# Kernel tuning notes

Hardware: AMD Instinct MI355X
Metric: run time of the kernel (lower is better)

Reference implementation:

```python
import jax, jax.numpy as jnp
import numpy as np

B, T, D = 64, 2048, 300

def setup_inputs() -> dict:
    key = jax.random.key(0)
    k1, k2, k3, k4 = jax.random.split(key, 4)
    gate_encoding = jax.random.uniform(k1, (B, T, D), dtype=jnp.float32)
    inputs_encoding = jax.random.normal(k2, (B, T, D), dtype=jnp.float32)
    # kaiming-normal-ish init: std = sqrt(2 / fan_in)
    std = float(np.sqrt(2.0 / D))
    Wz = jax.random.normal(k3, (D, D), dtype=jnp.float32) * std
    Wo = jax.random.normal(k4, (D, D), dtype=jnp.float32) * std
    bz = jnp.zeros((D,), dtype=jnp.float32)
    bo = jnp.zeros((D,), dtype=jnp.float32)
    return {"gate_encoding": gate_encoding, "inputs_encoding": inputs_encoding,
            "Wz": Wz, "bz": bz, "Wo": Wo, "bo": bo}

def reference(gate_encoding, inputs_encoding, Wz, bz, Wo, bo):
    # Batch the two linear projections across all timesteps (torch.nn.Linear: x @ W.T + b)
    z = jnp.tanh(jnp.einsum('btd,ed->bte', inputs_encoding, Wz) + bz)  # [B,T,D]
    o = jnp.tanh(jnp.einsum('btd,ed->bte', inputs_encoding, Wo) + bo)  # [B,T,D]

    # Sequential gated recurrence: c_t = g_t * c_{t-1} + (1 - g_t) * z_t ; h_t = o_t * c_t
    def step(c, gz_o):
        g_t, z_t, o_t = gz_o
        c = g_t * c + (1.0 - g_t) * z_t
        return c, o_t * c

    c0 = jnp.zeros((gate_encoding.shape[0], gate_encoding.shape[2]), dtype=inputs_encoding.dtype)
    # scan over time: move T to leading axis
    _, h = jax.lax.scan(step, c0,
                        (jnp.swapaxes(gate_encoding, 0, 1),
                         jnp.swapaxes(z, 0, 1),
                         jnp.swapaxes(o, 0, 1)))
    return jnp.swapaxes(h, 0, 1)  # [B,T,D]
```

## Files before the change

kernel.cpp:

```cpp
#include <hip/hip_runtime.h>
#include <hip/hip_bf16.h>

typedef _Float16 f16x8 __attribute__((ext_vector_type(8)));
typedef _Float16 f16x4 __attribute__((ext_vector_type(4)));
typedef float f32x4 __attribute__((ext_vector_type(4)));

#define B_SZ 64
#define T_SZ 2048
#define D_SZ 300
#define M_SZ (B_SZ * T_SZ)
#define KP 320
#define NP 640
#define NCHUNK 32
#define CLEN 64

__device__ __forceinline__ void gld_lds16(const void* g, void* l) {
    __builtin_amdgcn_global_load_lds(
        (const __attribute__((address_space(1))) unsigned int*)g,
        (__attribute__((address_space(3))) unsigned int*)l,
        16, 0, 0);
}

__device__ __forceinline__ float fast_tanh(float x) {
    float e = __expf(2.0f * x);
    return 1.0f - 2.0f * __builtin_amdgcn_rcpf(e + 1.0f);
}

__global__ void pack_x(const float* __restrict__ in, _Float16* __restrict__ out) {
    unsigned int i = blockIdx.x * 256u + threadIdx.x;
    f32x4 v = *(const f32x4*)(in + (size_t)i * 4);
#pragma unroll
    for (int j = 0; j < 4; ++j) {
        unsigned int f = i * 4 + j;
        unsigned int row = f / D_SZ;
        unsigned int k = f - row * D_SZ;
        out[(size_t)row * KP + k] = (_Float16)v[j];
    }
}

__global__ void pad_x(_Float16* __restrict__ out) {
    unsigned int i = blockIdx.x * 256u + threadIdx.x;
    unsigned int j = i * 4;
    unsigned int row = j / 20;
    unsigned int k0 = j - row * 20;
    f16x4 z = {};
    *(f16x4*)(out + (size_t)row * KP + 300 + k0) = z;
}

__global__ void pack_w(const float* __restrict__ Wz, const float* __restrict__ Wo,
                       _Float16* __restrict__ W) {
    unsigned int i = blockIdx.x * 256u + threadIdx.x;
    if (i >= NP * KP) return;
    unsigned int n = i / KP;
    unsigned int k = i - n * KP;
    float v = 0.0f;
    if (k < D_SZ) {
        if (n < D_SZ) v = Wz[n * D_SZ + k];
        else if (n >= 320 && n < 320 + D_SZ) v = Wo[(n - 320) * D_SZ + k];
    }
    W[i] = (_Float16)v;
}

__global__ void pack_bias(const float* __restrict__ bz, const float* __restrict__ bo,
                          float* __restrict__ bias) {
    int n = threadIdx.x;
    float v = 0.0f;
    if (n < D_SZ) v = bz[n];
    else if (n >= 320 && n < 320 + D_SZ) v = bo[n - 320];
    bias[n] = v;
}

__global__ __launch_bounds__(256) void gemm_zo(const _Float16* __restrict__ X,
                                               const _Float16* __restrict__ W,
                                               const float* __restrict__ bias,
                                               _Float16* __restrict__ C) {
    __shared__ _Float16 As[3][128 * 32];
    __shared__ _Float16 Bs[3][128 * 32];

    const int tid = threadIdx.x;
    const int lane = tid & 63;
    const int wid = tid >> 6;
    const int wm = wid >> 1, wn = wid & 1;

    int g = blockIdx.x;
    int s = (g & 7) * (5120 / 8) + (g >> 3);
    int bm = s / 5;
    int bn = s - bm * 5;

    f32x4 acc[4][4] = {};

    const int r_in_c = lane >> 2;
    const int u_phys = lane & 3;

    const _Float16* Abase = X + (size_t)(bm * 128) * KP;
    const _Float16* Bbase = W + (size_t)(bn * 128) * KP;

    auto stage = [&](int buf, int kt) {
#pragma unroll
        for (int j = 0; j < 2; ++j) {
            int c = wid + j * 4;
            int row = c * 16 + r_in_c;
            int ul = u_phys ^ ((row >> 1) & 3);
            gld_lds16(Abase + (size_t)row * KP + kt * 32 + ul * 8, &As[buf][c * 512]);
            gld_lds16(Bbase + (size_t)row * KP + kt * 32 + ul * 8, &Bs[buf][c * 512]);
        }
    };

    stage(0, 0);
    stage(1, 1);

#pragma unroll 1
    for (int kt = 0; kt < 10; ++kt) {
        if (kt < 8) {
            stage((kt + 2) % 3, kt + 2);
            asm volatile("s_waitcnt vmcnt(8)" ::: "memory");
        } else if (kt == 8) {
            asm volatile("s_waitcnt vmcnt(4)" ::: "memory");
        } else {
            asm volatile("s_waitcnt vmcnt(0)" ::: "memory");
        }
        __builtin_amdgcn_s_barrier();
        __builtin_amdgcn_sched_barrier(0);

        const int cb = kt % 3;
        f16x8 bf[4], af[4];
#pragma unroll
        for (int ns = 0; ns < 4; ++ns) {
            int row = wn * 64 + ns * 16 + (lane & 15);
            int u = (lane >> 4) ^ ((row >> 1) & 3);
            bf[ns] = *(const f16x8*)&Bs[cb][row * 32 + u * 8];
        }
#pragma unroll
        for (int ms = 0; ms < 4; ++ms) {
            int row = wm * 64 + ms * 16 + (lane & 15);
            int u = (lane >> 4) ^ ((row >> 1) & 3);
            af[ms] = *(const f16x8*)&As[cb][row * 32 + u * 8];
        }
        asm volatile("s_waitcnt lgkmcnt(0)" ::: "memory");
        __builtin_amdgcn_s_barrier();
        __builtin_amdgcn_sched_barrier(0);

        __builtin_amdgcn_s_setprio(1);
#pragma unroll
        for (int ms = 0; ms < 4; ++ms)
#pragma unroll
            for (int ns = 0; ns < 4; ++ns)
                acc[ms][ns] = __builtin_amdgcn_mfma_f32_16x16x32_f16(bf[ns], af[ms], acc[ms][ns], 0, 0, 0);
        __builtin_amdgcn_s_setprio(0);
    }

    const int mrow0 = bm * 128 + wm * 64;
    const int ncol0 = bn * 128 + wn * 64;
#pragma unroll
    for (int ns = 0; ns < 4; ++ns) {
        int nb = ncol0 + ns * 16 + (lane >> 4) * 4;
        f32x4 b4 = *(const f32x4*)&bias[nb];
#pragma unroll
        for (int ms = 0; ms < 4; ++ms) {
            int m = mrow0 + ms * 16 + (lane & 15);
            f16x4 v;
#pragma unroll
            for (int r = 0; r < 4; ++r)
                v[r] = (_Float16)fast_tanh(acc[ms][ns][r] + b4[r]);
            *(f16x4*)&C[(size_t)m * NP + nb] = v;
        }
    }
}

__global__ void scan_p1(const float* __restrict__ gate, const _Float16* __restrict__ C,
                        float* __restrict__ Aout, float* __restrict__ Bout) {
    int b = blockIdx.x >> 5;
    int nc = blockIdx.x & 31;
    int d = threadIdx.x;
    if (d >= D_SZ) return;
    size_t base = (size_t)b * T_SZ + (size_t)nc * CLEN;
    const float* gp = gate + base * D_SZ + d;
    const _Float16* zp = C + base * NP + d;
    float A = 1.0f, Bc = 0.0f;
    for (int t = 0; t < CLEN; ++t) {
        float gv = gp[(size_t)t * D_SZ];
        float zv = (float)zp[(size_t)t * NP];
        A *= gv;
        Bc = gv * Bc + (1.0f - gv) * zv;
    }
    int o = (b * NCHUNK + nc) * D_SZ + d;
    Aout[o] = A;
    Bout[o] = Bc;
}

__global__ void scan_p2(const float* __restrict__ A, const float* __restrict__ Bc,
                        float* __restrict__ Cin) {
    int idx = blockIdx.x * 256 + threadIdx.x;
    if (idx >= B_SZ * D_SZ) return;
    int b = idx / D_SZ;
    int d = idx - b * D_SZ;
    float c = 0.0f;
    for (int nc = 0; nc < NCHUNK; ++nc) {
        int o = (b * NCHUNK + nc) * D_SZ + d;
        Cin[o] = c;
        c = A[o] * c + Bc[o];
    }
}

__global__ void scan_p3(const float* __restrict__ gate, const _Float16* __restrict__ C,
                        const float* __restrict__ Cin, float* __restrict__ out) {
    int b = blockIdx.x >> 5;
    int nc = blockIdx.x & 31;
    int d = threadIdx.x;
    if (d >= D_SZ) return;
    size_t base = (size_t)b * T_SZ + (size_t)nc * CLEN;
    const float* gp = gate + base * D_SZ + d;
    const _Float16* zp = C + base * NP + d;
    const _Float16* op = zp + 320;
    float* hp = out + base * D_SZ + d;
    float c = Cin[(b * NCHUNK + nc) * D_SZ + d];
    for (int t = 0; t < CLEN; ++t) {
        float gv = gp[(size_t)t * D_SZ];
        float zv = (float)zp[(size_t)t * NP];
        float ov = (float)op[(size_t)t * NP];
        c = gv * c + (1.0f - gv) * zv;
        hp[(size_t)t * D_SZ] = ov * c;
    }
}

extern "C" void kernel_launch(void* const* d_in, const int* in_sizes, int n_in,
                              void* d_out, int out_size, void* d_ws, size_t ws_size,
                              hipStream_t stream) {
    const float* gate = (const float*)d_in[0];
    const float* xin  = (const float*)d_in[1];
    const float* Wz   = (const float*)d_in[2];
    const float* bz   = (const float*)d_in[3];
    const float* Wo   = (const float*)d_in[4];
    const float* bo   = (const float*)d_in[5];
    float* out = (float*)d_out;

    char* ws = (char*)d_ws;
    _Float16* Xf16 = (_Float16*)(ws);
    _Float16* C16  = (_Float16*)(ws + 83886080ull);
    _Float16* Wc   = (_Float16*)(ws + 251658240ull);
    float*    bias = (float*)   (ws + 252067840ull);
    float*    Ach  = (float*)   (ws);
    float*    Bch  = (float*)   (ws + 2457600ull);
    float*    Cin  = (float*)   (ws + 4915200ull);

    pack_x<<<(M_SZ * D_SZ / 4) / 256, 256, 0, stream>>>(xin, Xf16);
    pad_x<<<(M_SZ * 20 / 4) / 256, 256, 0, stream>>>(Xf16);
    pack_w<<<(NP * KP + 255) / 256, 256, 0, stream>>>(Wz, Wo, Wc);
    pack_bias<<<1, NP, 0, stream>>>(bz, bo, bias);

    gemm_zo<<<(M_SZ / 128) * (NP / 128), 256, 0, stream>>>(Xf16, Wc, bias, C16);

    scan_p1<<<B_SZ * NCHUNK, 320, 0, stream>>>(gate, C16, Ach, Bch);
    scan_p2<<<(B_SZ * D_SZ + 255) / 256, 256, 0, stream>>>(Ach, Bch, Cin);
    scan_p3<<<B_SZ * NCHUNK, 320, 0, stream>>>(gate, C16, Cin, out);
}
```

Measured before the change: 327.4 us.

## Fuse fp32-to-fp16 input conversion into GEMM with direct register loads

Drops the separate pack_x and pad_x kernels. The GEMM now reads fp32 X directly from global memory into registers and converts it to fp16 on the fly, masking the K tail past 300. The LDS staging, swizzling and barriers are replaced by per-wave register double-buffered global loads. This removes a full write and read pass of the packed f16 input. In exchange, the GEMM reads twice as many bytes per A element, waves sharing the same rows load them redundantly, and it loses LDS-based reuse.

```diff
diff --git a/kernel.cpp b/kernel.cpp
--- a/kernel.cpp
+++ b/kernel.cpp
@@ -14,37 +14,9 @@
 #define NCHUNK 32
 #define CLEN 64
 
-__device__ __forceinline__ void gld_lds16(const void* g, void* l) {
-    __builtin_amdgcn_global_load_lds(
-        (const __attribute__((address_space(1))) unsigned int*)g,
-        (__attribute__((address_space(3))) unsigned int*)l,
-        16, 0, 0);
-}
-
 __device__ __forceinline__ float fast_tanh(float x) {
     float e = __expf(2.0f * x);
     return 1.0f - 2.0f * __builtin_amdgcn_rcpf(e + 1.0f);
-}
-
-__global__ void pack_x(const float* __restrict__ in, _Float16* __restrict__ out) {
-    unsigned int i = blockIdx.x * 256u + threadIdx.x;
-    f32x4 v = *(const f32x4*)(in + (size_t)i * 4);
-#pragma unroll
-    for (int j = 0; j < 4; ++j) {
-        unsigned int f = i * 4 + j;
-        unsigned int row = f / D_SZ;
-        unsigned int k = f - row * D_SZ;
-        out[(size_t)row * KP + k] = (_Float16)v[j];
-    }
-}
-
-__global__ void pad_x(_Float16* __restrict__ out) {
-    unsigned int i = blockIdx.x * 256u + threadIdx.x;
-    unsigned int j = i * 4;
-    unsigned int row = j / 20;
-    unsigned int k0 = j - row * 20;
-    f16x4 z = {};
-    *(f16x4*)(out + (size_t)row * KP + 300 + k0) = z;
 }
 
 __global__ void pack_w(const float* __restrict__ Wz, const float* __restrict__ Wo,
@@ -70,16 +42,33 @@
     bias[n] = v;
 }
 
-__global__ __launch_bounds__(256) void gemm_zo(const _Float16* __restrict__ X,
+__device__ __forceinline__ f16x8 cvt8(f32x4 v0, f32x4 v1) {
+    f16x8 r;
+    r[0] = (_Float16)v0[0]; r[1] = (_Float16)v0[1];
+    r[2] = (_Float16)v0[2]; r[3] = (_Float16)v0[3];
+    r[4] = (_Float16)v1[0]; r[5] = (_Float16)v1[1];
+    r[6] = (_Float16)v1[2]; r[7] = (_Float16)v1[3];
+    return r;
+}
+
+__device__ __forceinline__ f16x8 loadA(const float* __restrict__ p, bool tail, int kq) {
+    f32x4 v0 = {}, v1 = {};
+    if (!tail) {
+        v0 = *(const f32x4*)p;
+        v1 = *(const f32x4*)(p + 4);
+    } else {
+        if (kq < 2) v0 = *(const f32x4*)p;
+        if (kq < 1) v1 = *(const f32x4*)(p + 4);
+    }
+    return cvt8(v0, v1);
+}
+
+__global__ __launch_bounds__(256) void gemm_zo(const float* __restrict__ X,
                                                const _Float16* __restrict__ W,
                                                const float* __restrict__ bias,
                                                _Float16* __restrict__ C) {
-    __shared__ _Float16 As[3][128 * 32];
-    __shared__ _Float16 Bs[3][128 * 32];
-
-    const int tid = threadIdx.x;
-    const int lane = tid & 63;
-    const int wid = tid >> 6;
+    const int lane = threadIdx.x & 63;
+    const int wid = threadIdx.x >> 6;
     const int wm = wid >> 1, wn = wid & 1;
 
     int g = blockIdx.x;
@@ -87,77 +76,66 @@
     int bm = s / 5;
     int bn = s - bm * 5;
 
+    const int l15 = lane & 15;
+    const int kq = lane >> 4;
+
+    const float* ap[4];
+    const _Float16* bp[4];
+#pragma unroll
+    for (int ms = 0; ms < 4; ++ms) {
+        int row = bm * 128 + wm * 64 + ms * 16 + l15;
+        ap[ms] = X + (size_t)row * D_SZ + kq * 8;
+    }
+#pragma unroll
+    for (int ns = 0; ns < 4; ++ns) {
+        int row = bn * 128 + wn * 64 + ns * 16 + l15;
+        bp[ns] = W + (size_t)row * KP + kq * 8;
+    }
+
     f32x4 acc[4][4] = {};
 
-    const int r_in_c = lane >> 2;
-    const int u_phys = lane & 3;
-
-    const _Float16* Abase = X + (size_t)(bm * 128) * KP;
-    const _Float16* Bbase = W + (size_t)(bn * 128) * KP;
-
-    auto stage = [&](int buf, int kt) {
-#pragma unroll
-        for (int j = 0; j < 2; ++j) {
-            int c = wid + j * 4;
-            int row = c * 16 + r_in_c;
-            int ul = u_phys ^ ((row >> 1) & 3);
-            gld_lds16(Abase + (size_t)row * KP + kt * 32 + ul * 8, &As[buf][c * 512]);
-            gld_lds16(Bbase + (size_t)row * KP + kt * 32 + ul * 8, &Bs[buf][c * 512]);
+    f16x8 ac[4], bc[4];
+#pragma unroll
+    for (int ms = 0; ms < 4; ++ms) ac[ms] = loadA(ap[ms], false, kq);
+#pragma unroll
+    for (int ns = 0; ns < 4; ++ns) bc[ns] = *(const f16x8*)(bp[ns]);
+
+#pragma unroll 2
+    for (int kt = 0; kt < 10; ++kt) {
+        f16x8 an[4], bnx[4];
+        if (kt < 9) {
+            bool tail = (kt == 8);
+#pragma unroll
+            for (int ms = 0; ms < 4; ++ms) an[ms] = loadA(ap[ms] + (kt + 1) * 32, tail, kq);
+#pragma unroll
+            for (int ns = 0; ns < 4; ++ns) bnx[ns] = *(const f16x8*)(bp[ns] + (kt + 1) * 32);
         }
-    };
-
-    stage(0, 0);
-    stage(1, 1);
-
-#pragma unroll 1
-    for (int kt = 0; kt < 10; ++kt) {
-        if (kt < 8) {
-            stage((kt + 2) % 3, kt + 2);
-            asm volatile("s_waitcnt vmcnt(8)" ::: "memory");
-        } else if (kt == 8) {
-            asm volatile("s_waitcnt vmcnt(4)" ::: "memory");
-        } else {
-            asm volatile("s_waitcnt vmcnt(0)" ::: "memory");
+
+        __builtin_amdgcn_s_setprio(1);
+#pragma unroll
+        for (int ms = 0; ms < 4; ++ms)
+#pragma unroll
+            for (int ns = 0; ns < 4; ++ns)
+                acc[ms][ns] = __builtin_amdgcn_mfma_f32_16x16x32_f16(bc[ns], ac[ms], acc[ms][ns], 0, 0, 0);
+        __builtin_amdgcn_s_setprio(0);
+
+        if (kt < 9) {
+#pragma unroll
+            for (int ms = 0; ms < 4; ++ms) ac[ms] = an[ms];
+#pragma unroll
+            for (int ns = 0; ns < 4; ++ns) bc[ns] = bnx[ns];
         }
-        __builtin_amdgcn_s_barrier();
-        __builtin_amdgcn_sched_barrier(0);
-
-        const int cb = kt % 3;
-        f16x8 bf[4], af[4];
-#pragma unroll
-        for (int ns = 0; ns < 4; ++ns) {
-            int row = wn * 64 + ns * 16 + (lane & 15);
-            int u = (lane >> 4) ^ ((row >> 1) & 3);
-            bf[ns] = *(const f16x8*)&Bs[cb][row * 32 + u * 8];
-        }
-#pragma unroll
-        for (int ms = 0; ms < 4; ++ms) {
-            int row = wm * 64 + ms * 16 + (lane & 15);
-            int u = (lane >> 4) ^ ((row >> 1) & 3);
-            af[ms] = *(const f16x8*)&As[cb][row * 32 + u * 8];
-        }
-        asm volatile("s_waitcnt lgkmcnt(0)" ::: "memory");
-        __builtin_amdgcn_s_barrier();
-        __builtin_amdgcn_sched_barrier(0);
-
-        __builtin_amdgcn_s_setprio(1);
-#pragma unroll
-        for (int ms = 0; ms < 4; ++ms)
-#pragma unroll
-            for (int ns = 0; ns < 4; ++ns)
-                acc[ms][ns] = __builtin_amdgcn_mfma_f32_16x16x32_f16(bf[ns], af[ms], acc[ms][ns], 0, 0, 0);
-        __builtin_amdgcn_s_setprio(0);
     }
 
     const int mrow0 = bm * 128 + wm * 64;
     const int ncol0 = bn * 128 + wn * 64;
 #pragma unroll
     for (int ns = 0; ns < 4; ++ns) {
-        int nb = ncol0 + ns * 16 + (lane >> 4) * 4;
+        int nb = ncol0 + ns * 16 + kq * 4;
         f32x4 b4 = *(const f32x4*)&bias[nb];
 #pragma unroll
         for (int ms = 0; ms < 4; ++ms) {
-            int m = mrow0 + ms * 16 + (lane & 15);
+            int m = mrow0 + ms * 16 + l15;
             f16x4 v;
 #pragma unroll
             for (int r = 0; r < 4; ++r)
@@ -235,20 +213,17 @@
     float* out = (float*)d_out;
 
     char* ws = (char*)d_ws;
-    _Float16* Xf16 = (_Float16*)(ws);
-    _Float16* C16  = (_Float16*)(ws + 83886080ull);
-    _Float16* Wc   = (_Float16*)(ws + 251658240ull);
-    float*    bias = (float*)   (ws + 252067840ull);
-    float*    Ach  = (float*)   (ws);
-    float*    Bch  = (float*)   (ws + 2457600ull);
-    float*    Cin  = (float*)   (ws + 4915200ull);
-
-    pack_x<<<(M_SZ * D_SZ / 4) / 256, 256, 0, stream>>>(xin, Xf16);
-    pad_x<<<(M_SZ * 20 / 4) / 256, 256, 0, stream>>>(Xf16);
+    _Float16* C16  = (_Float16*)(ws);
+    _Float16* Wc   = (_Float16*)(ws + 167772160ull);
+    float*    bias = (float*)   (ws + 168181760ull);
+    float*    Ach  = (float*)   (ws + 168184320ull);
+    float*    Bch  = (float*)   (ws + 170641920ull);
+    float*    Cin  = (float*)   (ws + 173099520ull);
+
     pack_w<<<(NP * KP + 255) / 256, 256, 0, stream>>>(Wz, Wo, Wc);
     pack_bias<<<1, NP, 0, stream>>>(bz, bo, bias);
 
-    gemm_zo<<<(M_SZ / 128) * (NP / 128), 256, 0, stream>>>(Xf16, Wc, bias, C16);
+    gemm_zo<<<(M_SZ / 128) * (NP / 128), 256, 0, stream>>>(xin, Wc, bias, C16);
 
     scan_p1<<<B_SZ * NCHUNK, 320, 0, stream>>>(gate, C16, Ach, Bch);
     scan_p2<<<(B_SZ * D_SZ + 255) / 256, 256, 0, stream>>>(Ach, Bch, Cin);
```

Result: slower. 415.8 us (+27.0%).

## Merge X pack and pad kernels; stage GEMM epilogue through LDS for wide stores

Applied to the files above, without the earlier changes.

The fp16 packing of X now runs in one kernel: each thread converts a row-aligned group of four floats into an f16x4 store, or zero-fills the padding, replacing scalar half stores and a separate pad launch. The GEMM epilogue writes tanh results into a swizzled per-wave LDS tile, then reads them back as 16-byte rows, so global stores to C are coalesced 128-byte row segments instead of scattered 8-byte writes. This adds a barrier and LDS round-trips in the epilogue.

```diff
diff --git a/kernel.cpp b/kernel.cpp
--- a/kernel.cpp
+++ b/kernel.cpp
@@ -28,23 +28,18 @@
 
 __global__ void pack_x(const float* __restrict__ in, _Float16* __restrict__ out) {
     unsigned int i = blockIdx.x * 256u + threadIdx.x;
-    f32x4 v = *(const f32x4*)(in + (size_t)i * 4);
-#pragma unroll
-    for (int j = 0; j < 4; ++j) {
-        unsigned int f = i * 4 + j;
-        unsigned int row = f / D_SZ;
-        unsigned int k = f - row * D_SZ;
-        out[(size_t)row * KP + k] = (_Float16)v[j];
-    }
-}
-
-__global__ void pad_x(_Float16* __restrict__ out) {
-    unsigned int i = blockIdx.x * 256u + threadIdx.x;
-    unsigned int j = i * 4;
-    unsigned int row = j / 20;
-    unsigned int k0 = j - row * 20;
-    f16x4 z = {};
-    *(f16x4*)(out + (size_t)row * KP + 300 + k0) = z;
+    unsigned int row = i / 80;
+    unsigned int kq = i - row * 80;
+    if (kq < 75) {
+        f32x4 v = *(const f32x4*)(in + (size_t)row * D_SZ + kq * 4);
+        f16x4 h;
+#pragma unroll
+        for (int r = 0; r < 4; ++r) h[r] = (_Float16)v[r];
+        *(f16x4*)(out + (size_t)row * KP + kq * 4) = h;
+    } else {
+        f16x4 z = {};
+        *(f16x4*)(out + (size_t)row * KP + 300 + (kq - 75) * 4) = z;
+    }
 }
 
 __global__ void pack_w(const float* __restrict__ Wz, const float* __restrict__ Wo,
@@ -109,6 +104,9 @@
     stage(0, 0);
     stage(1, 1);
 
+    const int l15 = lane & 15;
+    const int kq = lane >> 4;
+
 #pragma unroll 1
     for (int kt = 0; kt < 10; ++kt) {
         if (kt < 8) {
@@ -126,14 +124,14 @@
         f16x8 bf[4], af[4];
 #pragma unroll
         for (int ns = 0; ns < 4; ++ns) {
-            int row = wn * 64 + ns * 16 + (lane & 15);
-            int u = (lane >> 4) ^ ((row >> 1) & 3);
+            int row = wn * 64 + ns * 16 + l15;
+            int u = kq ^ ((row >> 1) & 3);
             bf[ns] = *(const f16x8*)&Bs[cb][row * 32 + u * 8];
         }
 #pragma unroll
         for (int ms = 0; ms < 4; ++ms) {
-            int row = wm * 64 + ms * 16 + (lane & 15);
-            int u = (lane >> 4) ^ ((row >> 1) & 3);
+            int row = wm * 64 + ms * 16 + l15;
+            int u = kq ^ ((row >> 1) & 3);
             af[ms] = *(const f16x8*)&As[cb][row * 32 + u * 8];
         }
         asm volatile("s_waitcnt lgkmcnt(0)" ::: "memory");
@@ -149,20 +147,35 @@
         __builtin_amdgcn_s_setprio(0);
     }
 
+    __syncthreads();
+    _Float16* et = &As[0][0] + wid * 1024;
+
     const int mrow0 = bm * 128 + wm * 64;
     const int ncol0 = bn * 128 + wn * 64;
-#pragma unroll
-    for (int ns = 0; ns < 4; ++ns) {
-        int nb = ncol0 + ns * 16 + (lane >> 4) * 4;
-        f32x4 b4 = *(const f32x4*)&bias[nb];
-#pragma unroll
-        for (int ms = 0; ms < 4; ++ms) {
-            int m = mrow0 + ms * 16 + (lane & 15);
+    const int row8 = lane >> 3;
+    const int u8 = lane & 7;
+
+    f32x4 b4[4];
+#pragma unroll
+    for (int ns = 0; ns < 4; ++ns)
+        b4[ns] = *(const f32x4*)&bias[ncol0 + ns * 16 + kq * 4];
+
+#pragma unroll
+    for (int ms = 0; ms < 4; ++ms) {
+#pragma unroll
+        for (int ns = 0; ns < 4; ++ns) {
             f16x4 v;
 #pragma unroll
             for (int r = 0; r < 4; ++r)
-                v[r] = (_Float16)fast_tanh(acc[ms][ns][r] + b4[r]);
-            *(f16x4*)&C[(size_t)m * NP + nb] = v;
+                v[r] = (_Float16)fast_tanh(acc[ms][ns][r] + b4[ns][r]);
+            int up = ((ns << 1) | (kq >> 1)) ^ (l15 & 7);
+            *(f16x4*)&et[l15 * 64 + up * 8 + (kq & 1) * 4] = v;
+        }
+#pragma unroll
+        for (int j = 0; j < 2; ++j) {
+            int rr = row8 + j * 8;
+            f16x8 o = *(const f16x8*)&et[rr * 64 + (u8 ^ (rr & 7)) * 8];
+            *(f16x8*)&C[(size_t)(mrow0 + ms * 16 + rr) * NP + ncol0 + u8 * 8] = o;
         }
     }
 }
@@ -243,8 +256,7 @@
     float*    Bch  = (float*)   (ws + 2457600ull);
     float*    Cin  = (float*)   (ws + 4915200ull);
 
-    pack_x<<<(M_SZ * D_SZ / 4) / 256, 256, 0, stream>>>(xin, Xf16);
-    pad_x<<<(M_SZ * 20 / 4) / 256, 256, 0, stream>>>(Xf16);
+    pack_x<<<(M_SZ * 80) / 256, 256, 0, stream>>>(xin, Xf16);
     pack_w<<<(NP * KP + 255) / 256, 256, 0, stream>>>(Wz, Wo, Wc);
     pack_bias<<<1, NP, 0, stream>>>(bz, bo, bias);
 
```

Result: faster. 304.1 us (-7.1%).
